# Kernel optimization log

Measured on AMD Instinct MI355X. Metric: run time of the kernel, lower is better.

Reference implementation:

```python
import jax, jax.numpy as jnp
import numpy as np

DIM = 768
HEADS = 12
HD = DIM // HEADS
SCALE = float(np.sqrt(HD))  # sqrt(dim // num_heads)


def layernorm(x, g, b, eps=1e-5):
    m = jnp.mean(x, axis=-1, keepdims=True)
    v = jnp.var(x, axis=-1, keepdims=True)
    return (x - m) * jax.lax.rsqrt(v + eps) * g + b


def dwconv(x, w, b, pad):
    # x: [B,C,H,W], w: [C,1,kh,kw] depthwise
    y = jax.lax.conv_general_dilated(
        x, w, window_strides=(1, 1), padding=[(pad, pad), (pad, pad)],
        feature_group_count=x.shape[1], dimension_numbers=('NCHW', 'OIHW', 'NCHW'))
    return y + b[None, :, None, None]


def mha(xq, xkv, wq, bq, wk, bk, wv, bv, wo, bo):
    # per-head Linears batched over heads; wq/wk/wv: [H, C, hd], biases [H, hd]
    B, N, C = xq.shape
    q = jnp.einsum('bnc,hcd->bhnd', xq, wq) + bq[None, :, None, :]
    k = jnp.einsum('bnc,hcd->bhnd', xkv, wk) + bk[None, :, None, :]
    v = jnp.einsum('bnc,hcd->bhnd', xkv, wv) + bv[None, :, None, :]
    z = jax.nn.sigmoid(jnp.einsum('bhnd,bhmd->bhnm', q, k) / SCALE)  # sigmoid, not softmax
    o = jnp.einsum('bhnm,bhmd->bhnd', z, v)
    o = o.transpose(0, 2, 1, 3).reshape(B, N, C)  # concat heads along feature dim
    return o @ wo + bo


def reference(decoder, wq1, bq1, wk1, bk1, wv1, bv1, wo1, bo1,
              wq2, bq2, wk2, bk2, wv2, bv2, wo2, bo2,
              alphas1, alphas2, peg_w, peg_b,
              ln1_g, ln1_b, ln2_g, ln2_b,
              cn_dw_w, cn_dw_b, cn_ln_g, cn_ln_b,
              cn_w1, cn_b1, cn_w2, cn_b2, cn_scale, cn_alphas):
    B, C, H, W = decoder.shape
    x = decoder.transpose(0, 2, 3, 1).reshape(B, H * W, C)  # [B,N,C]
    # block 1: alpha * x + MHA(x,x,x)
    x = alphas1 * x + mha(x, x, wq1, bq1, wk1, bk1, wv1, bv1, wo1, bo1)
    # PEG: depthwise 3x3 conv (replaces x, no residual in source)
    x4 = x.reshape(B, H, W, C).transpose(0, 3, 1, 2)
    x4 = dwconv(x4, peg_w, peg_b, pad=1)
    x = x4.transpose(0, 2, 3, 1).reshape(B, H * W, C)
    x = layernorm(x, ln1_g, ln1_b)
    # block 2 (encoder is None -> self-attention)
    x = alphas2 * x + mha(x, x, wq2, bq2, wk2, bk2, wv2, bv2, wo2, bo2)
    x = layernorm(x, ln2_g, ln2_b)
    x4 = x.reshape(B, H, W, C).transpose(0, 3, 1, 2)  # [B,C,H,W]
    # CNBlock head: dwconv7x7 -> LN -> Linear(4d) -> GELU -> Linear(d), layer_scale + alpha residual
    y = dwconv(x4, cn_dw_w, cn_dw_b, pad=3)
    y = y.transpose(0, 2, 3, 1)  # [B,H,W,C]
    y = layernorm(y, cn_ln_g, cn_ln_b)
    y = jax.nn.gelu(y @ cn_w1 + cn_b1, approximate=False)
    y = y @ cn_w2 + cn_b2
    y = y.transpose(0, 3, 1, 2)  # [B,C,H,W]
    out = cn_scale[None, :, None, None] * y + x4 * cn_alphas[None, :, None, None]
    return out


def setup_inputs() -> dict:
    key = jax.random.key(0)
    ks = iter(jax.random.split(key, 40))
    def n(shape, s=0.02):
        return jax.random.normal(next(ks), shape, dtype=jnp.float32) * s
    d = {}
    d['decoder'] = jax.random.normal(next(ks), (8, DIM, 32, 32), dtype=jnp.float32)
    for i in (1, 2):
        d[f'wq{i}'] = n((HEADS, DIM, HD)); d[f'bq{i}'] = n((HEADS, HD), 1e-6)
        d[f'wk{i}'] = n((HEADS, DIM, HD)); d[f'bk{i}'] = n((HEADS, HD), 1e-6)
        d[f'wv{i}'] = n((HEADS, DIM, HD)); d[f'bv{i}'] = n((HEADS, HD), 1e-6)
        d[f'wo{i}'] = n((DIM, DIM)); d[f'bo{i}'] = n((DIM,), 1e-6)
    d['alphas1'] = jnp.ones((DIM,), jnp.float32)
    d['alphas2'] = jnp.ones((DIM,), jnp.float32)
    d['peg_w'] = n((DIM, 1, 3, 3), 0.1); d['peg_b'] = n((DIM,), 1e-6)
    d['ln1_g'] = jnp.ones((DIM,), jnp.float32); d['ln1_b'] = jnp.zeros((DIM,), jnp.float32)
    d['ln2_g'] = jnp.ones((DIM,), jnp.float32); d['ln2_b'] = jnp.zeros((DIM,), jnp.float32)
    d['cn_dw_w'] = n((DIM, 1, 7, 7), 0.1); d['cn_dw_b'] = n((DIM,), 0.02)
    d['cn_ln_g'] = jnp.ones((DIM,), jnp.float32); d['cn_ln_b'] = jnp.zeros((DIM,), jnp.float32)
    d['cn_w1'] = n((DIM, 4 * DIM)); d['cn_b1'] = n((4 * DIM,), 0.02)
    d['cn_w2'] = n((4 * DIM, DIM)); d['cn_b2'] = n((DIM,), 0.02)
    d['cn_scale'] = jnp.full((DIM,), 1e-6, jnp.float32)
    d['cn_alphas'] = jnp.ones((DIM,), jnp.float32)
    return d
```

## Files before the change

kernel.cpp:

```cpp
#include <hip/hip_runtime.h>
#include <math.h>

#define BATCH 8
#define CDIM 768
#define NTOK 1024
#define NH 12
#define HDIM 64

typedef __attribute__((ext_vector_type(8))) short bf16x8;
typedef __attribute__((ext_vector_type(4))) float f32x4;

__device__ inline short f2bf(float f) {
    union { float f; unsigned u; } v; v.f = f;
    unsigned r = (v.u + 0x7FFF + ((v.u >> 16) & 1)) >> 16;
    return (short)r;
}

__device__ inline void async_copy16(const short* g, short* l) {
    __builtin_amdgcn_global_load_lds(
        (const __attribute__((address_space(1))) void*)g,
        (__attribute__((address_space(3))) void*)l, 16, 0, 0);
}

__global__ void k_transpose_in(const float* __restrict__ dec, float* __restrict__ x,
                               short* __restrict__ xb) {
    __shared__ float tile[32][33];
    int b = blockIdx.z;
    int n0 = blockIdx.x * 32;
    int c0 = blockIdx.y * 32;
    int tx = threadIdx.x, ty = threadIdx.y;
#pragma unroll
    for (int r = 0; r < 4; ++r) {
        int c = c0 + ty + r * 8;
        tile[ty + r * 8][tx] = dec[((size_t)b * CDIM + c) * NTOK + n0 + tx];
    }
    __syncthreads();
#pragma unroll
    for (int r = 0; r < 4; ++r) {
        int n = n0 + ty + r * 8;
        float val = tile[tx][ty + r * 8];
        size_t idx = ((size_t)b * NTOK + n) * CDIM + c0 + tx;
        x[idx] = val;
        xb[idx] = f2bf(val);
    }
}

__global__ void k_wtrans(const float* __restrict__ src, short* __restrict__ dst,
                         int R, int C) {
    __shared__ float tile[32][33];
    int c0 = blockIdx.x * 32, r0 = blockIdx.y * 32;
    int tx = threadIdx.x, ty = threadIdx.y;
#pragma unroll
    for (int p = 0; p < 4; ++p)
        tile[ty + p * 8][tx] = src[(size_t)(r0 + ty + p * 8) * C + c0 + tx];
    __syncthreads();
#pragma unroll
    for (int p = 0; p < 4; ++p)
        dst[(size_t)(c0 + ty + p * 8) * R + r0 + tx] = f2bf(tile[tx][ty + p * 8]);
}

__global__ __launch_bounds__(256) void k_packqkv(
    const float* __restrict__ wq1, const float* __restrict__ wk1, const float* __restrict__ wv1,
    const float* __restrict__ wq2, const float* __restrict__ wk2, const float* __restrict__ wv2,
    short* __restrict__ dst1, short* __restrict__ dst2) {
    __shared__ float tile[64][65];
    int z = blockIdx.y;
    int set = z / 36, rem = z % 36, sect = rem / 12, h = rem % 12;
    const float* srcs[6] = {wq1, wk1, wv1, wq2, wk2, wv2};
    const float* src = srcs[set * 3 + sect] + (size_t)h * 768 * 64;
    short* dst = (set ? dst2 : dst1) + ((size_t)sect * 768 + h * 64) * 768;
    int k0 = blockIdx.x * 64;
    int t = threadIdx.x;
#pragma unroll
    for (int p = 0; p < 16; ++p) {
        int gid = t + p * 256;
        int r = gid >> 6, c = gid & 63;
        tile[r][c] = src[(size_t)(k0 + r) * 64 + c];
    }
    __syncthreads();
#pragma unroll
    for (int p = 0; p < 16; ++p) {
        int gid = t + p * 256;
        int d = gid >> 6, kk = gid & 63;
        dst[(size_t)d * 768 + k0 + kk] = f2bf(tile[kk][d]);
    }
}

__global__ void k_packbias(const float* __restrict__ bq1, const float* __restrict__ bk1,
                           const float* __restrict__ bv1, const float* __restrict__ bq2,
                           const float* __restrict__ bk2, const float* __restrict__ bv2,
                           float* __restrict__ d1, float* __restrict__ d2) {
    int tid = blockIdx.x * 256 + threadIdx.x;
    if (tid >= 4608) return;
    int set = tid / 2304, n = tid % 2304;
    int sect = n / 768, rem = n % 768;
    const float* srcs[6] = {bq1, bk1, bv1, bq2, bk2, bv2};
    float v = srcs[set * 3 + sect][rem];
    (set ? d2 : d1)[n] = v;
}

#define GM_FINAL 0
#define GM_PROJ  1
#define GM_GELU  2
#define GM_QKV   3
#define QKVSEC ((size_t)BATCH * NH * NTOK * HDIM)

template<int MODE, int BN>
__global__ __launch_bounds__(256) void k_gemm_mfma(
    const short* __restrict__ A, const short* __restrict__ Bt,
    const float* __restrict__ bias, const float* __restrict__ resid,
    const float* __restrict__ rscale, const float* __restrict__ alph,
    float* __restrict__ outF, short* __restrict__ outB, int M, int N, int K) {
    constexpr int NT = BN / 32;
    constexpr int BP = BN / 64;
    constexpr int STAGE = 2 * 128 * 32 + 2 * BN * 32;
    constexpr int FINALS = (MODE == GM_FINAL) ? 64 * 132 * 2 : 0;
    constexpr int SMEM = STAGE > FINALS ? STAGE : FINALS;
    __shared__ short smem[SMEM];
    short* As = smem;
    short* Bs = smem + 2 * 128 * 32;
    int t = threadIdx.x;
    int w = t >> 6, lane = t & 63, l15 = lane & 15, quad = lane >> 4;
    int r0 = blockIdx.x * 128, n0 = blockIdx.y * BN;
    int wr = (w >> 1) * 64, wc = (w & 1) * (BN / 2);
    f32x4 acc[4][NT];
#pragma unroll
    for (int i = 0; i < 4; ++i)
#pragma unroll
        for (int j = 0; j < NT; ++j) acc[i][j] = (f32x4){0.f, 0.f, 0.f, 0.f};
    int sr = t >> 2, sc = (t & 3) * 8;
    const short* Ag = A + (size_t)(r0 + sr) * K + sc;
    const short* Bg = Bt + (size_t)(n0 + sr) * K + sc;
    short* AsW = As + w * 512;
    short* BsW = Bs + w * 512;
    for (int k0 = 0; k0 < K; k0 += 64) {
        __syncthreads();
#pragma unroll
        for (int c = 0; c < 2; ++c) {
#pragma unroll
            for (int p = 0; p < 2; ++p)
                async_copy16(Ag + k0 + c * 32 + (size_t)p * 64 * K,
                             AsW + c * 4096 + p * 2048);
#pragma unroll
            for (int p = 0; p < BP; ++p)
                async_copy16(Bg + k0 + c * 32 + (size_t)p * 64 * K,
                             BsW + c * (BN * 32) + p * 2048);
        }
        __syncthreads();
#pragma unroll
        for (int c = 0; c < 2; ++c) {
            bf16x8 af[4], bf[NT];
#pragma unroll
            for (int i = 0; i < 4; ++i)
                af[i] = *(const bf16x8*)&As[c * 4096 + (wr + i * 16 + l15) * 32 + quad * 8];
#pragma unroll
            for (int j = 0; j < NT; ++j)
                bf[j] = *(const bf16x8*)&Bs[c * (BN * 32) + (wc + j * 16 + l15) * 32 + quad * 8];
#pragma unroll
            for (int i = 0; i < 4; ++i)
#pragma unroll
                for (int j = 0; j < NT; ++j)
                    acc[i][j] = __builtin_amdgcn_mfma_f32_16x16x32_bf16(af[i], bf[j], acc[i][j], 0, 0, 0);
        }
    }
    if (MODE == GM_FINAL) {
        __syncthreads();
        float* T = (float*)smem;
#pragma unroll
        for (int i = 0; i < 4; ++i)
#pragma unroll
            for (int j = 0; j < NT; ++j)
#pragma unroll
                for (int rr = 0; rr < 4; ++rr) {
                    int rl = wr + i * 16 + quad * 4 + rr;
                    int cl = wc + j * 16 + l15;
                    int row = r0 + rl, col = n0 + cl;
                    float val = acc[i][j][rr] + bias[col];
                    val = rscale[col] * val + alph[col] * resid[(size_t)row * N + col];
                    T[cl * 132 + rl] = val;
                }
        __syncthreads();
        int c = t >> 2, qo = (t & 3) * 32;
        int b = r0 >> 10, tokbase = r0 & 1023;
        float* obase = outF + ((size_t)(b * 768 + n0 + c)) * 1024 + tokbase + qo;
#pragma unroll
        for (int ii = 0; ii < 8; ++ii)
            *(float4*)&obase[ii * 4] = *(float4*)&T[c * 132 + qo + ii * 4];
        return;
    }
#pragma unroll
    for (int i = 0; i < 4; ++i)
#pragma unroll
        for (int j = 0; j < NT; ++j)
#pragma unroll
            for (int rr = 0; rr < 4; ++rr) {
                int row = r0 + wr + i * 16 + quad * 4 + rr;
                int col = n0 + wc + j * 16 + l15;
                float val = acc[i][j][rr] + bias[col];
                if (MODE == GM_PROJ) {
                    val += rscale[col] * resid[(size_t)row * N + col];
                    outF[(size_t)row * N + col] = val;
                } else if (MODE == GM_GELU) {
                    float u = val * (1.0f + 0.044715f * val * val);
                    float zz = __builtin_amdgcn_rcpf(
                        1.0f + __builtin_amdgcn_exp2f(-2.3022082f * u));
                    outB[(size_t)row * N + col] = f2bf(val * zz);
                } else {
                    int sect = col / 768, rem = col - sect * 768;
                    int hh = rem >> 6, d = rem & 63;
                    int bb = row >> 10, tok = row & 1023;
                    outB[(size_t)sect * QKVSEC +
                         (((size_t)bb * NH + hh) * NTOK + tok) * HDIM + d] = f2bf(val);
                }
            }
}

__global__ __launch_bounds__(256) void k_attn_mfma(
    const short* __restrict__ q, const short* __restrict__ k,
    const short* __restrict__ v, short* __restrict__ o) {
    __shared__ short Ks[64][72];
    __shared__ short Vt[64][72];
    __shared__ short Ps[128][72];
    int b = blockIdx.z, h = blockIdx.y;
    int q0 = blockIdx.x * 128;
    int t = threadIdx.x;
    int w = t >> 6, lane = t & 63, l15 = lane & 15, quad = lane >> 4;
    size_t base = ((size_t)(b * NH + h)) * NTOK * HDIM;
    const short* qp = q + base;
    const short* kp = k + base;
    const short* vp = v + base;
    bf16x8 qf[2][2];
#pragma unroll
    for (int mt = 0; mt < 2; ++mt)
#pragma unroll
        for (int kc = 0; kc < 2; ++kc)
            qf[mt][kc] = *(const bf16x8*)&qp[(size_t)(q0 + w * 32 + mt * 16 + l15) * HDIM + kc * 32 + quad * 8];
    f32x4 oacc[2][4];
#pragma unroll
    for (int mt = 0; mt < 2; ++mt)
#pragma unroll
        for (int dt = 0; dt < 4; ++dt) oacc[mt][dt] = (f32x4){0.f, 0.f, 0.f, 0.f};
    for (int kt = 0; kt < 16; ++kt) {
        __syncthreads();
#pragma unroll
        for (int p = 0; p < 2; ++p) {
            int gid = t + p * 256;
            int r = gid >> 3, c8 = (gid & 7) * 8;
            *(bf16x8*)&Ks[r][c8] = *(const bf16x8*)&kp[(size_t)(kt * 64 + r) * HDIM + c8];
        }
#pragma unroll
        for (int p = 0; p < 2; ++p) {
            int tok = t & 63, d0 = (t >> 6) * 8 + p * 32;
            bf16x8 vv = *(const bf16x8*)&vp[(size_t)(kt * 64 + tok) * HDIM + d0];
#pragma unroll
            for (int j = 0; j < 8; ++j) Vt[d0 + j][tok] = vv[j];
        }
        __syncthreads();
        f32x4 sacc[2][4];
#pragma unroll
        for (int mt = 0; mt < 2; ++mt)
#pragma unroll
            for (int nt = 0; nt < 4; ++nt) sacc[mt][nt] = (f32x4){0.f, 0.f, 0.f, 0.f};
#pragma unroll
        for (int nt = 0; nt < 4; ++nt) {
            bf16x8 kf0 = *(const bf16x8*)&Ks[nt * 16 + l15][quad * 8];
            bf16x8 kf1 = *(const bf16x8*)&Ks[nt * 16 + l15][32 + quad * 8];
#pragma unroll
            for (int mt = 0; mt < 2; ++mt) {
                sacc[mt][nt] = __builtin_amdgcn_mfma_f32_16x16x32_bf16(qf[mt][0], kf0, sacc[mt][nt], 0, 0, 0);
                sacc[mt][nt] = __builtin_amdgcn_mfma_f32_16x16x32_bf16(qf[mt][1], kf1, sacc[mt][nt], 0, 0, 0);
            }
        }
#pragma unroll
        for (int mt = 0; mt < 2; ++mt)
#pragma unroll
            for (int nt = 0; nt < 4; ++nt)
#pragma unroll
                for (int rr = 0; rr < 4; ++rr) {
                    float s = sacc[mt][nt][rr];
                    float z = __builtin_amdgcn_rcpf(
                        1.0f + __builtin_amdgcn_exp2f(s * -0.18033688011112042f));
                    Ps[w * 32 + mt * 16 + quad * 4 + rr][nt * 16 + l15] = f2bf(z);
                }
        __syncthreads();
        bf16x8 vfr[2][4];
#pragma unroll
        for (int kc = 0; kc < 2; ++kc)
#pragma unroll
            for (int dt = 0; dt < 4; ++dt)
                vfr[kc][dt] = *(const bf16x8*)&Vt[dt * 16 + l15][kc * 32 + quad * 8];
#pragma unroll
        for (int mt = 0; mt < 2; ++mt)
#pragma unroll
            for (int kc = 0; kc < 2; ++kc) {
                bf16x8 pf = *(const bf16x8*)&Ps[w * 32 + mt * 16 + l15][kc * 32 + quad * 8];
#pragma unroll
                for (int dt = 0; dt < 4; ++dt)
                    oacc[mt][dt] = __builtin_amdgcn_mfma_f32_16x16x32_bf16(pf, vfr[kc][dt], oacc[mt][dt], 0, 0, 0);
            }
    }
#pragma unroll
    for (int mt = 0; mt < 2; ++mt)
#pragma unroll
        for (int dt = 0; dt < 4; ++dt)
#pragma unroll
            for (int rr = 0; rr < 4; ++rr) {
                int tok = q0 + w * 32 + mt * 16 + quad * 4 + rr;
                int c = h * 64 + dt * 16 + l15;
                o[((size_t)b * NTOK + tok) * CDIM + c] = f2bf(oacc[mt][dt][rr]);
            }
}

template<int K>
__global__ __launch_bounds__(256) void k_dwconv_t(
    const float* __restrict__ in, const float* __restrict__ w,
    const float* __restrict__ bias, float* __restrict__ out) {
    constexpr int PAD = K / 2;
    constexpr int KK = K * K;
    int t = threadIdx.x;
    int c = blockIdx.y * 64 + (t & 63);
    int j = blockIdx.x * 4 + (t >> 6);
    int b = blockIdx.z;
    float wr[KK];
#pragma unroll
    for (int qq = 0; qq < KK; ++qq) wr[qq] = w[(size_t)c * KK + qq];
    float bsv = bias[c];
    const float* base = in + (size_t)b * NTOK * CDIM + c;
    float win[K][K];
#pragma unroll
    for (int s = 1; s < K; ++s) {
        int ii = s - 1 - PAD;
#pragma unroll
        for (int qq = 0; qq < K; ++qq) {
            int jj = j - PAD + qq;
            win[s][qq] = (ii >= 0 && jj >= 0 && jj < 32)
                         ? base[(size_t)(ii * 32 + jj) * CDIM] : 0.0f;
        }
    }
#pragma unroll
    for (int i = 0; i < 32; ++i) {
#pragma unroll
        for (int r = 0; r < K - 1; ++r)
#pragma unroll
            for (int qq = 0; qq < K; ++qq) win[r][qq] = win[r + 1][qq];
        int ii = i + PAD;
#pragma unroll
        for (int qq = 0; qq < K; ++qq) {
            int jj = j - PAD + qq;
            win[K - 1][qq] = (ii < 32 && jj >= 0 && jj < 32)
                             ? base[(size_t)(ii * 32 + jj) * CDIM] : 0.0f;
        }
        float acc = bsv;
#pragma unroll
        for (int r = 0; r < K; ++r)
#pragma unroll
            for (int qq = 0; qq < K; ++qq)
                acc = fmaf(win[r][qq], wr[r * K + qq], acc);
        out[((size_t)b * NTOK + i * 32 + j) * CDIM + c] = acc;
    }
}

__global__ __launch_bounds__(256) void k_ln(
    const float* __restrict__ in, const float* __restrict__ g,
    const float* __restrict__ b, float* __restrict__ outF, short* __restrict__ outB) {
    int row = blockIdx.x;
    const float* xr = in + (size_t)row * CDIM;
    int t = threadIdx.x;
    float x0 = xr[t], x1 = xr[t + 256], x2 = xr[t + 512];
    float s = x0 + x1 + x2;
    float sq = x0 * x0 + x1 * x1 + x2 * x2;
#pragma unroll
    for (int off = 32; off > 0; off >>= 1) {
        s += __shfl_down(s, off);
        sq += __shfl_down(sq, off);
    }
    __shared__ float ws[4], wq2[4];
    int wid = t >> 6, lane = t & 63;
    if (lane == 0) { ws[wid] = s; wq2[wid] = sq; }
    __syncthreads();
    if (t == 0) {
        float S = ws[0] + ws[1] + ws[2] + ws[3];
        float Q = wq2[0] + wq2[1] + wq2[2] + wq2[3];
        float m = S * (1.0f / CDIM);
        float var = Q * (1.0f / CDIM) - m * m;
        ws[0] = m;
        wq2[0] = rsqrtf(var + 1e-5f);
    }
    __syncthreads();
    float m = ws[0], inv = wq2[0];
    float y0 = (x0 - m) * inv * g[t] + b[t];
    float y1 = (x1 - m) * inv * g[t + 256] + b[t + 256];
    float y2 = (x2 - m) * inv * g[t + 512] + b[t + 512];
    if (outF) {
        float* orow = outF + (size_t)row * CDIM;
        orow[t] = y0; orow[t + 256] = y1; orow[t + 512] = y2;
    }
    if (outB) {
        short* orow = outB + (size_t)row * CDIM;
        orow[t] = f2bf(y0); orow[t + 256] = f2bf(y1); orow[t + 512] = f2bf(y2);
    }
}

extern "C" void kernel_launch(void* const* d_in, const int* in_sizes, int n_in,
                              void* d_out, int out_size, void* d_ws, size_t ws_size,
                              hipStream_t stream) {
    const float* dec = (const float*)d_in[0];
    const float* wq1 = (const float*)d_in[1]; const float* bq1 = (const float*)d_in[2];
    const float* wk1 = (const float*)d_in[3]; const float* bk1 = (const float*)d_in[4];
    const float* wv1 = (const float*)d_in[5]; const float* bv1 = (const float*)d_in[6];
    const float* wo1 = (const float*)d_in[7]; const float* bo1 = (const float*)d_in[8];
    const float* wq2 = (const float*)d_in[9]; const float* bq2 = (const float*)d_in[10];
    const float* wk2 = (const float*)d_in[11]; const float* bk2 = (const float*)d_in[12];
    const float* wv2 = (const float*)d_in[13]; const float* bv2 = (const float*)d_in[14];
    const float* wo2 = (const float*)d_in[15]; const float* bo2 = (const float*)d_in[16];
    const float* alphas1 = (const float*)d_in[17];
    const float* alphas2 = (const float*)d_in[18];
    const float* peg_w = (const float*)d_in[19]; const float* peg_b = (const float*)d_in[20];
    const float* ln1_g = (const float*)d_in[21]; const float* ln1_b = (const float*)d_in[22];
    const float* ln2_g = (const float*)d_in[23]; const float* ln2_b = (const float*)d_in[24];
    const float* cn_dw_w = (const float*)d_in[25]; const float* cn_dw_b = (const float*)d_in[26];
    const float* cn_ln_g = (const float*)d_in[27]; const float* cn_ln_b = (const float*)d_in[28];
    const float* cn_w1 = (const float*)d_in[29]; const float* cn_b1 = (const float*)d_in[30];
    const float* cn_w2 = (const float*)d_in[31]; const float* cn_b2 = (const float*)d_in[32];
    const float* cn_scale = (const float*)d_in[33]; const float* cn_alphas = (const float*)d_in[34];
    float* out = (float*)d_out;

    const size_t S = (size_t)BATCH * NTOK * CDIM;
    float* A0 = (float*)d_ws;
    float* A1 = A0 + S;
    short* Xb  = (short*)(A1 + S);
    short* QKV = Xb + S;
    short* Ob  = QKV + 3 * S;
    short* Hb  = Ob + S;
    short* Wqkv1 = Hb + 2 * S;
    short* Wqkv2 = Wqkv1 + 2304 * 768;
    short* WoT1  = Wqkv2 + 2304 * 768;
    short* WoT2  = WoT1 + 768 * 768;
    short* W1T   = WoT2 + 768 * 768;
    short* W2T   = W1T + (size_t)3072 * 768;
    float* bqkv1 = (float*)(W2T + (size_t)768 * 3072);
    float* bqkv2 = bqkv1 + 2304;
    short* Hfull = QKV + 2 * S;

    dim3 tb(32, 8);
    dim3 dwgrid(8, 12, 8);

    k_packqkv<<<dim3(12, 72), 256, 0, stream>>>(wq1, wk1, wv1, wq2, wk2, wv2, Wqkv1, Wqkv2);
    k_wtrans<<<dim3(24, 24), tb, 0, stream>>>(wo1, WoT1, 768, 768);
    k_wtrans<<<dim3(24, 24), tb, 0, stream>>>(wo2, WoT2, 768, 768);
    k_wtrans<<<dim3(96, 24), tb, 0, stream>>>(cn_w1, W1T, 768, 3072);
    k_wtrans<<<dim3(24, 96), tb, 0, stream>>>(cn_w2, W2T, 3072, 768);
    k_packbias<<<18, 256, 0, stream>>>(bq1, bk1, bv1, bq2, bk2, bv2, bqkv1, bqkv2);

    k_transpose_in<<<dim3(32, 24, 8), tb, 0, stream>>>(dec, A0, Xb);

    k_gemm_mfma<GM_QKV, 128><<<dim3(64, 18), 256, 0, stream>>>(
        Xb, Wqkv1, bqkv1, nullptr, nullptr, nullptr, nullptr, QKV, 8192, 2304, 768);
    k_attn_mfma<<<dim3(8, 12, 8), 256, 0, stream>>>(QKV, QKV + S, QKV + 2 * S, Ob);
    k_gemm_mfma<GM_PROJ, 64><<<dim3(64, 12), 256, 0, stream>>>(
        Ob, WoT1, bo1, A0, alphas1, nullptr, A1, nullptr, 8192, 768, 768);
    k_dwconv_t<3><<<dwgrid, 256, 0, stream>>>(A1, peg_w, peg_b, A0);
    k_ln<<<8192, 256, 0, stream>>>(A0, ln1_g, ln1_b, A1, Xb);

    k_gemm_mfma<GM_QKV, 128><<<dim3(64, 18), 256, 0, stream>>>(
        Xb, Wqkv2, bqkv2, nullptr, nullptr, nullptr, nullptr, QKV, 8192, 2304, 768);
    k_attn_mfma<<<dim3(8, 12, 8), 256, 0, stream>>>(QKV, QKV + S, QKV + 2 * S, Ob);
    k_gemm_mfma<GM_PROJ, 64><<<dim3(64, 12), 256, 0, stream>>>(
        Ob, WoT2, bo2, A1, alphas2, nullptr, A0, nullptr, 8192, 768, 768);
    k_ln<<<8192, 256, 0, stream>>>(A0, ln2_g, ln2_b, A1, nullptr);

    k_dwconv_t<7><<<dwgrid, 256, 0, stream>>>(A1, cn_dw_w, cn_dw_b, A0);
    k_ln<<<8192, 256, 0, stream>>>(A0, cn_ln_g, cn_ln_b, nullptr, Xb);
    k_gemm_mfma<GM_GELU, 128><<<dim3(64, 24), 256, 0, stream>>>(
        Xb, W1T, cn_b1, nullptr, nullptr, nullptr, nullptr, Hfull, 8192, 3072, 768);
    k_gemm_mfma<GM_FINAL, 64><<<dim3(64, 12), 256, 0, stream>>>(
        Hfull, W2T, cn_b2, A1, cn_scale, cn_alphas, out, nullptr, 8192, 768, 3072);
}
```

Baseline: 651.1 us.

## Double-buffer GEMM K-loop with async LDS prefetch of next slice

Restructures the bf16 MFMA GEMM main loop from loading a 64-wide K chunk then computing into a ping-pong scheme over 32-wide K slices. The next slice is issued with global_load_lds into the alternate LDS buffer before the MFMAs run on the current one, so the load wait no longer sits directly in front of compute. There is one barrier per slice instead of two per 64-wide chunk. Some leftover prologue code issues a redundant A copy and contains an empty loop, which adds a little wasted work.

```diff
diff --git a/kernel.cpp b/kernel.cpp
--- a/kernel.cpp
+++ b/kernel.cpp
@@ -133,35 +133,44 @@
     const short* Bg = Bt + (size_t)(n0 + sr) * K + sc;
     short* AsW = As + w * 512;
     short* BsW = Bs + w * 512;
-    for (int k0 = 0; k0 < K; k0 += 64) {
-        __syncthreads();
-#pragma unroll
-        for (int c = 0; c < 2; ++c) {
+#pragma unroll
+    for (int p = 0; p < 2; ++p)
+        async_copy16(Ag, AsW + p * 2048), Ag += (size_t)64 * K * 0;
+#pragma unroll
+    for (int p = 0; p < 2; ++p)
+        ;
+#pragma unroll
+    for (int p = 0; p < 2; ++p)
+        async_copy16(Ag + (size_t)p * 64 * K, AsW + p * 2048);
+#pragma unroll
+    for (int p = 0; p < BP; ++p)
+        async_copy16(Bg + (size_t)p * 64 * K, BsW + p * 2048);
+    int st = 0;
+    for (int k0 = 0; k0 < K; k0 += 32, st ^= 1) {
+        __syncthreads();
+        if (k0 + 32 < K) {
+            int nst = st ^ 1;
 #pragma unroll
             for (int p = 0; p < 2; ++p)
-                async_copy16(Ag + k0 + c * 32 + (size_t)p * 64 * K,
-                             AsW + c * 4096 + p * 2048);
+                async_copy16(Ag + k0 + 32 + (size_t)p * 64 * K,
+                             AsW + nst * 4096 + p * 2048);
 #pragma unroll
             for (int p = 0; p < BP; ++p)
-                async_copy16(Bg + k0 + c * 32 + (size_t)p * 64 * K,
-                             BsW + c * (BN * 32) + p * 2048);
-        }
-        __syncthreads();
-#pragma unroll
-        for (int c = 0; c < 2; ++c) {
-            bf16x8 af[4], bf[NT];
-#pragma unroll
-            for (int i = 0; i < 4; ++i)
-                af[i] = *(const bf16x8*)&As[c * 4096 + (wr + i * 16 + l15) * 32 + quad * 8];
+                async_copy16(Bg + k0 + 32 + (size_t)p * 64 * K,
+                             BsW + nst * (BN * 32) + p * 2048);
+        }
+        bf16x8 af[4], bf[NT];
+#pragma unroll
+        for (int i = 0; i < 4; ++i)
+            af[i] = *(const bf16x8*)&As[st * 4096 + (wr + i * 16 + l15) * 32 + quad * 8];
+#pragma unroll
+        for (int j = 0; j < NT; ++j)
+            bf[j] = *(const bf16x8*)&Bs[st * (BN * 32) + (wc + j * 16 + l15) * 32 + quad * 8];
+#pragma unroll
+        for (int i = 0; i < 4; ++i)
 #pragma unroll
             for (int j = 0; j < NT; ++j)
-                bf[j] = *(const bf16x8*)&Bs[c * (BN * 32) + (wc + j * 16 + l15) * 32 + quad * 8];
-#pragma unroll
-            for (int i = 0; i < 4; ++i)
-#pragma unroll
-                for (int j = 0; j < NT; ++j)
-                    acc[i][j] = __builtin_amdgcn_mfma_f32_16x16x32_bf16(af[i], bf[j], acc[i][j], 0, 0, 0);
-        }
+                acc[i][j] = __builtin_amdgcn_mfma_f32_16x16x32_bf16(af[i], bf[j], acc[i][j], 0, 0, 0);
     }
     if (MODE == GM_FINAL) {
         __syncthreads();
```

New measurement: 622.4 us. 1.05x faster.
